# Kernel optimization log

Measured on AMD Instinct MI355X. Metric: run time of the kernel, lower is better.

Reference implementation:

```python
import jax, jax.numpy as jnp
import numpy as np

B, S, D, H = 1, 2048, 2048, 32
HD = D // H
SCALE = float(HD) ** -0.5


def _rope(x, cos, sin):
    # x: (b, s, h, hd); interleaved-pair RoPE as in executorch apply_rotary_emb
    xr, xi = x[..., 0::2], x[..., 1::2]
    c = cos[None, :, None, :]
    s = sin[None, :, None, :]
    out = jnp.stack([xr * c - xi * s, xr * s + xi * c], axis=-1)
    return out.reshape(x.shape)


def setup_inputs() -> dict:
    key = jax.random.key(0)
    ks = jax.random.split(key, 8)
    hidden_states = jax.random.normal(ks[0], (B, S, D), jnp.float32)
    pos = jnp.arange(S, dtype=jnp.float32)
    inv = 1.0 / (10000.0 ** (jnp.arange(0, HD, 2, dtype=jnp.float32) / HD))
    ang = pos[:, None] * inv[None, :]  # (S, HD//2)
    freqs_cos = jnp.cos(ang)
    freqs_sin = jnp.sin(ang)
    causal = jnp.tril(jnp.ones((S, S), dtype=bool))
    attention_mask = jnp.where(causal, 0.0, -1e9).astype(jnp.float32)[None, None]
    k_cache = jax.random.normal(ks[1], (B, S, H, HD), jnp.float32)
    v_cache = jax.random.normal(ks[2], (B, S, H, HD), jnp.float32)
    k_mask = jnp.ones((B, S, 1, 1), jnp.float32)
    v_mask = jnp.ones((B, S, 1, 1), jnp.float32)
    # weights stored as (in, out); math-equivalent to torch Linear(out,in) @ W.T
    wq = jax.random.normal(ks[3], (D, D), jnp.float32) * 0.02
    wk = jax.random.normal(ks[4], (D, D), jnp.float32) * 0.02
    wv = jax.random.normal(ks[5], (D, D), jnp.float32) * 0.02
    wo = jax.random.normal(ks[6], (D, D), jnp.float32) * 0.02
    return {"hidden_states": hidden_states, "freqs_cos": freqs_cos,
            "freqs_sin": freqs_sin, "attention_mask": attention_mask,
            "k_cache": k_cache, "v_cache": v_cache,
            "k_mask": k_mask, "v_mask": v_mask,
            "wq": wq, "wk": wk, "wv": wv, "wo": wo}


def reference(hidden_states, freqs_cos, freqs_sin, attention_mask,
              k_cache, v_cache, k_mask, v_mask, wq, wk, wv, wo):
    b, s, _ = hidden_states.shape
    q = (hidden_states @ wq).reshape(b, s, H, HD)
    k = (hidden_states @ wk).reshape(b, s, H, HD)
    v = (hidden_states @ wv).reshape(b, s, H, HD)
    q = _rope(q, freqs_cos, freqs_sin)
    k = _rope(k, freqs_cos, freqs_sin)
    # mask-blend KV cache update
    k = k_cache * (1.0 - k_mask) + k * k_mask  # (b, S, H, HD)
    v = v_cache * (1.0 - v_mask) + v * v_mask
    qt = q.transpose(0, 2, 1, 3)  # (b, H, s, HD)
    kt = k.transpose(0, 2, 1, 3)
    vt = v.transpose(0, 2, 1, 3)
    attn = jnp.einsum('bhqd,bhkd->bhqk', qt, kt) * SCALE + attention_mask
    attn = jax.nn.softmax(attn, axis=-1)
    y = jnp.einsum('bhqk,bhkd->bhqd', attn, vt)  # (b, H, s, HD)
    # torch: y.transpose(0,1).contiguous().view(b, s, dim); valid since b == 1
    y = jnp.swapaxes(y, 0, 1).reshape(b, s, D)
    y = y @ wo
    return (y, k, v)
```

## Files before the change

kernel.cpp:

```cpp
#include <hip/hip_runtime.h>
#include <hip/hip_bf16.h>
#include <stdint.h>

typedef __bf16 bf16;
typedef __attribute__((ext_vector_type(8))) __bf16 bf16x8;
typedef __attribute__((ext_vector_type(4))) float f32x4;

#define SEQ 2048
#define DIM 2048
#define NHEAD 32
#define HD 64
#define ATT_SCALE 0.125f

__device__ __forceinline__ void gload16(void* lds, const void* g) {
  __builtin_amdgcn_global_load_lds(
      (const __attribute__((address_space(1))) unsigned int*)g,
      (__attribute__((address_space(3))) unsigned int*)lds, 16, 0, 0);
}

__device__ __forceinline__ f32x4 mfma16(bf16x8 a, bf16x8 b, f32x4 c) {
  return __builtin_amdgcn_mfma_f32_16x16x32_bf16(a, b, c, 0, 0, 0);
}

__global__ __launch_bounds__(256) void cvt_hs(const float* __restrict__ in,
                                              bf16* __restrict__ out) {
  size_t i = ((size_t)blockIdx.x * 256 + threadIdx.x) * 8;
  f32x4 a = *(const f32x4*)(in + i);
  f32x4 b = *(const f32x4*)(in + i + 4);
  bf16x8 o;
#pragma unroll
  for (int j = 0; j < 4; ++j) { o[j] = (bf16)a[j]; o[j + 4] = (bf16)b[j]; }
  *(bf16x8*)(out + i) = o;
}

__global__ __launch_bounds__(256) void wtrans(
    const float* __restrict__ w0, const float* __restrict__ w1,
    const float* __restrict__ w2, const float* __restrict__ w3,
    bf16* __restrict__ t0, bf16* __restrict__ t1,
    bf16* __restrict__ t2, bf16* __restrict__ t3) {
  const float* wsrc[4] = {w0, w1, w2, w3};
  bf16* wdst[4] = {t0, t1, t2, t3};
  const float* w = wsrc[blockIdx.z];
  bf16* wT = wdst[blockIdx.z];
  __shared__ alignas(16) bf16 tile[64][72];
  int t = threadIdx.x;
  int n0 = blockIdx.x * 64, k0 = blockIdx.y * 64;
#pragma unroll
  for (int i = 0; i < 4; ++i) {
    int r = (t >> 4) + 16 * i;
    int c = (t & 15) * 4;
    f32x4 v = *(const f32x4*)(w + (size_t)(k0 + r) * DIM + n0 + c);
#pragma unroll
    for (int j = 0; j < 4; ++j) tile[r][c + j] = (bf16)v[j];
  }
  __syncthreads();
#pragma unroll
  for (int i = 0; i < 2; ++i) {
    int n = (t >> 3) + 32 * i;
    int kb = (t & 7) * 8;
    bf16x8 o;
#pragma unroll
    for (int j = 0; j < 8; ++j) o[j] = tile[kb + j][n];
    *(bf16x8*)(wT + (size_t)(n0 + n) * DIM + k0 + kb) = o;
  }
}

template <typename OutT>
__global__ __launch_bounds__(256) void gemm128(
    const bf16* __restrict__ A,
    const bf16* __restrict__ B0, const bf16* __restrict__ B1, const bf16* __restrict__ B2,
    OutT* __restrict__ C0, OutT* __restrict__ C1, OutT* __restrict__ C2,
    int M, int N, int K) {
  const bf16* Bt; OutT* C;
  if (blockIdx.z == 0)      { Bt = B0; C = C0; }
  else if (blockIdx.z == 1) { Bt = B1; C = C1; }
  else                      { Bt = B2; C = C2; }
  __shared__ alignas(16) bf16 As[128][64];
  __shared__ alignas(16) bf16 Bs[128][64];
  int tid = threadIdx.x, lane = tid & 63, w = tid >> 6;
  int wr = w >> 1, wc = w & 1;
  size_t mBase = (size_t)blockIdx.y * 128, nBase = (size_t)blockIdx.x * 128;
  f32x4 acc[4][4] = {};
  int r0 = tid >> 3, sl = tid & 7;
  int lr = lane & 15, hi = lane >> 4, sw = lr & 7;
  for (int kt = 0; kt < K; kt += 64) {
#pragma unroll
    for (int i = 0; i < 4; ++i) {
      int row = r0 + 32 * i;
      int kc = sl ^ (row & 7);
      gload16(&As[row][sl * 8], A + (mBase + row) * K + kt + kc * 8);
      gload16(&Bs[row][sl * 8], Bt + (nBase + row) * K + kt + kc * 8);
    }
    __syncthreads();
#pragma unroll
    for (int kk = 0; kk < 2; ++kk) {
      int cb = kk * 4 + hi;
      bf16x8 a[4], b[4];
#pragma unroll
      for (int m = 0; m < 4; ++m)
        a[m] = *(const bf16x8*)&As[wr * 64 + m * 16 + lr][(cb ^ sw) * 8];
#pragma unroll
      for (int n = 0; n < 4; ++n)
        b[n] = *(const bf16x8*)&Bs[wc * 64 + n * 16 + lr][(cb ^ sw) * 8];
#pragma unroll
      for (int m = 0; m < 4; ++m)
#pragma unroll
        for (int n = 0; n < 4; ++n)
          acc[m][n] = mfma16(a[m], b[n], acc[m][n]);
    }
    __syncthreads();
  }
#pragma unroll
  for (int m = 0; m < 4; ++m)
#pragma unroll
    for (int n = 0; n < 4; ++n)
#pragma unroll
      for (int j = 0; j < 4; ++j) {
        size_t row = mBase + wr * 64 + m * 16 + hi * 4 + j;
        size_t col = nBase + wc * 64 + n * 16 + lr;
        C[row * N + col] = (OutT)acc[m][n][j];
      }
}

__global__ __launch_bounds__(256) void gemm_osk(
    const bf16* __restrict__ A, const bf16* __restrict__ Bt,
    float* __restrict__ P0, float* __restrict__ P1) {
  const int K = DIM, N = DIM;
  float* C = blockIdx.z ? P1 : P0;
  int kbeg = blockIdx.z * (K / 2), kend = kbeg + K / 2;
  __shared__ alignas(16) bf16 As[128][64];
  __shared__ alignas(16) bf16 Bs[128][64];
  int tid = threadIdx.x, lane = tid & 63, w = tid >> 6;
  int wr = w >> 1, wc = w & 1;
  size_t mBase = (size_t)blockIdx.y * 128, nBase = (size_t)blockIdx.x * 128;
  f32x4 acc[4][4] = {};
  int r0 = tid >> 3, sl = tid & 7;
  int lr = lane & 15, hi = lane >> 4, sw = lr & 7;
  for (int kt = kbeg; kt < kend; kt += 64) {
#pragma unroll
    for (int i = 0; i < 4; ++i) {
      int row = r0 + 32 * i;
      int kc = sl ^ (row & 7);
      gload16(&As[row][sl * 8], A + (mBase + row) * K + kt + kc * 8);
      gload16(&Bs[row][sl * 8], Bt + (nBase + row) * K + kt + kc * 8);
    }
    __syncthreads();
#pragma unroll
    for (int kk = 0; kk < 2; ++kk) {
      int cb = kk * 4 + hi;
      bf16x8 a[4], b[4];
#pragma unroll
      for (int m = 0; m < 4; ++m)
        a[m] = *(const bf16x8*)&As[wr * 64 + m * 16 + lr][(cb ^ sw) * 8];
#pragma unroll
      for (int n = 0; n < 4; ++n)
        b[n] = *(const bf16x8*)&Bs[wc * 64 + n * 16 + lr][(cb ^ sw) * 8];
#pragma unroll
      for (int m = 0; m < 4; ++m)
#pragma unroll
        for (int n = 0; n < 4; ++n)
          acc[m][n] = mfma16(a[m], b[n], acc[m][n]);
    }
    __syncthreads();
  }
#pragma unroll
  for (int m = 0; m < 4; ++m)
#pragma unroll
    for (int n = 0; n < 4; ++n)
#pragma unroll
      for (int j = 0; j < 4; ++j) {
        size_t row = mBase + wr * 64 + m * 16 + hi * 4 + j;
        size_t col = nBase + wc * 64 + n * 16 + lr;
        C[row * N + col] = acc[m][n][j];
      }
}

__global__ __launch_bounds__(256) void addp(const float* __restrict__ a,
                                            const float* __restrict__ b,
                                            float* __restrict__ y) {
  size_t i = ((size_t)blockIdx.x * 256 + threadIdx.x) * 4;
  f32x4 va = *(const f32x4*)(a + i);
  f32x4 vb = *(const f32x4*)(b + i);
  *(f32x4*)(y + i) = va + vb;
}

__global__ __launch_bounds__(256) void ropeqk(
    const bf16* __restrict__ qraw, const bf16* __restrict__ kraw,
    const float* __restrict__ fc, const float* __restrict__ fs,
    const float* __restrict__ kcache, const float* __restrict__ kmask,
    float* __restrict__ kout, bf16* __restrict__ qb, bf16* __restrict__ kb) {
  int s = blockIdx.x;
  float km = kmask[s];
  float omk = 1.0f - km;
  for (int p = threadIdx.x; p < DIM / 2; p += 256) {
    int h = p >> 5, i = p & 31;
    float c = fc[s * 32 + i], sn = fs[s * 32 + i];
    size_t src = (size_t)s * DIM + h * 64 + 2 * i;
    float xr = (float)qraw[src], xi = (float)qraw[src + 1];
    float q0v = xr * c - xi * sn, q1v = xr * sn + xi * c;
    size_t dsth = (size_t)h * SEQ * HD + (size_t)s * HD + 2 * i;
    qb[dsth] = (bf16)q0v; qb[dsth + 1] = (bf16)q1v;
    xr = (float)kraw[src]; xi = (float)kraw[src + 1];
    float k0v = xr * c - xi * sn, k1v = xr * sn + xi * c;
    float b0 = kcache[src] * omk + k0v * km;
    float b1 = kcache[src + 1] * omk + k1v * km;
    kout[src] = b0; kout[src + 1] = b1;
    kb[dsth] = (bf16)b0; kb[dsth + 1] = (bf16)b1;
  }
}

__global__ __launch_bounds__(256) void vprep(
    const bf16* __restrict__ vraw, const float* __restrict__ vcache,
    const float* __restrict__ vmask, float* __restrict__ vout,
    bf16* __restrict__ vtb) {
  int h = blockIdx.y;
  int s0 = blockIdx.x * 64;
  __shared__ alignas(16) bf16 tile[64][72];
  int t = threadIdx.x;
#pragma unroll
  for (int i = 0; i < 4; ++i) {
    int r = (t >> 4) + 16 * i;
    int c = (t & 15) * 4;
    int s = s0 + r;
    float vm = vmask[s], om = 1.0f - vm;
    size_t src = (size_t)s * DIM + h * 64 + c;
    f32x4 vc = *(const f32x4*)(vcache + src);
    f32x4 o;
#pragma unroll
    for (int j = 0; j < 4; ++j) {
      float val = vc[j] * om + (float)vraw[src + j] * vm;
      o[j] = val;
      tile[r][c + j] = (bf16)val;
    }
    *(f32x4*)(vout + src) = o;
  }
  __syncthreads();
#pragma unroll
  for (int i = 0; i < 2; ++i) {
    int hd = (t >> 3) + 32 * i;
    int cb = (t & 7) * 8;
    bf16x8 o;
#pragma unroll
    for (int j = 0; j < 8; ++j) o[j] = tile[cb + j][hd];
    *(bf16x8*)(vtb + (size_t)h * HD * SEQ + (size_t)hd * SEQ + s0 + cb) = o;
  }
}

__global__ __launch_bounds__(256) void attn_fwd(
    const bf16* __restrict__ qb, const bf16* __restrict__ kb,
    const bf16* __restrict__ vtb, bf16* __restrict__ ob) {
  int h = blockIdx.y;
  int qt = (h & 1) ? (31 - (int)blockIdx.x) : (int)blockIdx.x;
  int q0 = qt * 64;
  __shared__ alignas(16) bf16 Ks[2][64][64];
  __shared__ alignas(16) bf16 Vs[2][64][64];
  __shared__ alignas(16) bf16 Ps[4][16][64];
  int tid = threadIdx.x, lane = tid & 63, w = tid >> 6;
  const bf16* qh = qb + (size_t)h * SEQ * HD;
  const bf16* kh = kb + (size_t)h * SEQ * HD;
  const bf16* vh = vtb + (size_t)h * HD * SEQ;
  int lr = lane & 15, hi = lane >> 4, sw = lr & 7;
  int qrow = q0 + w * 16 + lr;
  bf16x8 qf[2];
#pragma unroll
  for (int kk = 0; kk < 2; ++kk)
    qf[kk] = *(const bf16x8*)(qh + (size_t)qrow * HD + kk * 32 + hi * 8);
  f32x4 ot[4] = {};
  float mrun = -3e38f, lrun = 0.f;
  int nt = qt + 1;
  int r0 = tid >> 3, sl = tid & 7;
  char* PsW = (char*)&Ps[w][0][0];

  auto STAGE = [&](int t, int b) {
    int kv0 = t * 64;
#pragma unroll
    for (int i = 0; i < 2; ++i) {
      int row = r0 + 32 * i;
      int kc = sl ^ (row & 7);
      gload16(&Ks[b][row][sl * 8], kh + (size_t)(kv0 + row) * HD + kc * 8);
      gload16(&Vs[b][row][sl * 8], vh + (size_t)row * SEQ + kv0 + kc * 8);
    }
  };

  STAGE(0, 0);
  int buf = 0;
  for (int t = 0; t < nt; ++t) {
    __syncthreads();
    if (t + 1 < nt) STAGE(t + 1, buf ^ 1);
    int kv0 = t * 64;
    f32x4 st[4] = {};
    __builtin_amdgcn_s_setprio(1);
#pragma unroll
    for (int kk = 0; kk < 2; ++kk) {
      int cb = kk * 4 + hi;
#pragma unroll
      for (int n = 0; n < 4; ++n) {
        bf16x8 kf = *(const bf16x8*)&Ks[buf][n * 16 + lr][(cb ^ sw) * 8];
        st[n] = mfma16(kf, qf[kk], st[n]);
      }
    }
    __builtin_amdgcn_s_setprio(0);
    float tmax = -3e38f;
    if (t == nt - 1) {
#pragma unroll
      for (int n = 0; n < 4; ++n)
#pragma unroll
        for (int j = 0; j < 4; ++j) {
          int key = kv0 + n * 16 + hi * 4 + j;
          float v = (key <= qrow) ? st[n][j] * ATT_SCALE : -1e30f;
          st[n][j] = v;
          tmax = fmaxf(tmax, v);
        }
    } else {
#pragma unroll
      for (int n = 0; n < 4; ++n)
#pragma unroll
        for (int j = 0; j < 4; ++j) {
          float v = st[n][j] * ATT_SCALE;
          st[n][j] = v;
          tmax = fmaxf(tmax, v);
        }
    }
    tmax = fmaxf(tmax, __shfl_xor(tmax, 16));
    tmax = fmaxf(tmax, __shfl_xor(tmax, 32));
    float mnew = fmaxf(mrun, tmax);
    float psum = 0.f;
    if (__all(tmax <= mrun)) {
#pragma unroll
      for (int n = 0; n < 4; ++n)
#pragma unroll
        for (int j = 0; j < 4; ++j) {
          float p = __expf(st[n][j] - mrun);
          st[n][j] = p;
          psum += p;
        }
      psum += __shfl_xor(psum, 16);
      psum += __shfl_xor(psum, 32);
      lrun += psum;
    } else {
      float alpha = __expf(mrun - mnew);
#pragma unroll
      for (int n = 0; n < 4; ++n)
#pragma unroll
        for (int j = 0; j < 4; ++j) {
          float p = __expf(st[n][j] - mnew);
          st[n][j] = p;
          psum += p;
        }
      psum += __shfl_xor(psum, 16);
      psum += __shfl_xor(psum, 32);
      lrun = lrun * alpha + psum;
      mrun = mnew;
#pragma unroll
      for (int nd = 0; nd < 4; ++nd)
#pragma unroll
        for (int j = 0; j < 4; ++j) ot[nd][j] *= alpha;
    }
#pragma unroll
    for (int n = 0; n < 4; ++n) {
      union { bf16 b[4]; uint2 u; } pk;
#pragma unroll
      for (int j = 0; j < 4; ++j) pk.b[j] = (bf16)st[n][j];
      int keyc = n * 2 + (hi >> 1);
      *(uint2*)(PsW + lr * 128 + ((keyc ^ sw) * 16) + (hi & 1) * 8) = pk.u;
    }
    __builtin_amdgcn_s_setprio(1);
#pragma unroll
    for (int kk = 0; kk < 2; ++kk) {
      int cb = kk * 4 + hi;
      bf16x8 pf = *(const bf16x8*)(PsW + lr * 128 + ((cb ^ sw) * 16));
#pragma unroll
      for (int nd = 0; nd < 4; ++nd) {
        bf16x8 vf = *(const bf16x8*)&Vs[buf][nd * 16 + lr][(cb ^ sw) * 8];
        ot[nd] = mfma16(vf, pf, ot[nd]);
      }
    }
    __builtin_amdgcn_s_setprio(0);
    buf ^= 1;
  }
  float rinv = 1.0f / lrun;
  bf16* orow = ob + ((size_t)h * SEQ + qrow) * HD;
#pragma unroll
  for (int nd = 0; nd < 4; ++nd) {
    union { bf16 b[4]; uint2 u; } o;
#pragma unroll
    for (int j = 0; j < 4; ++j) o.b[j] = (bf16)(ot[nd][j] * rinv);
    *(uint2*)(orow + nd * 16 + hi * 4) = o.u;
  }
}

extern "C" void kernel_launch(void* const* d_in, const int* in_sizes, int n_in,
                              void* d_out, int out_size, void* d_ws, size_t ws_size,
                              hipStream_t stream) {
  const float* hs     = (const float*)d_in[0];
  const float* fc     = (const float*)d_in[1];
  const float* fs     = (const float*)d_in[2];
  const float* kcache = (const float*)d_in[4];
  const float* vcache = (const float*)d_in[5];
  const float* kmask  = (const float*)d_in[6];
  const float* vmask  = (const float*)d_in[7];
  const float* wq     = (const float*)d_in[8];
  const float* wk     = (const float*)d_in[9];
  const float* wv     = (const float*)d_in[10];
  const float* wo     = (const float*)d_in[11];

  float* y    = (float*)d_out;
  float* kout = y + (size_t)SEQ * DIM;
  float* vout = y + 2 * (size_t)SEQ * DIM;

  char* ws = (char*)d_ws;
  const size_t MB8 = (size_t)SEQ * DIM * sizeof(bf16);
  bf16* wqT  = (bf16*)(ws + 0 * MB8);
  bf16* wkT  = (bf16*)(ws + 1 * MB8);
  bf16* wvT  = (bf16*)(ws + 2 * MB8);
  bf16* woT  = (bf16*)(ws + 3 * MB8);
  bf16* hsb  = (bf16*)(ws + 4 * MB8);
  bf16* qraw = (bf16*)(ws + 5 * MB8);
  bf16* kraw = (bf16*)(ws + 6 * MB8);
  bf16* vraw = (bf16*)(ws + 7 * MB8);
  bf16* qb   = (bf16*)(ws + 8 * MB8);
  bf16* kb   = (bf16*)(ws + 9 * MB8);
  bf16* vtb  = (bf16*)(ws + 10 * MB8);
  bf16* ob   = hsb;
  float* p0 = (float*)(ws + 5 * MB8);
  float* p1 = (float*)(ws + 7 * MB8);

  cvt_hs<<<dim3(SEQ * DIM / 2048), dim3(256), 0, stream>>>(hs, hsb);
  wtrans<<<dim3(32, 32, 4), dim3(256), 0, stream>>>(wq, wk, wv, wo, wqT, wkT, wvT, woT);
  gemm128<bf16><<<dim3(16, 16, 3), dim3(256), 0, stream>>>(
      hsb, wqT, wkT, wvT, qraw, kraw, vraw, SEQ, DIM, DIM);
  ropeqk<<<dim3(SEQ), dim3(256), 0, stream>>>(qraw, kraw, fc, fs, kcache, kmask, kout, qb, kb);
  vprep<<<dim3(32, 32), dim3(256), 0, stream>>>(vraw, vcache, vmask, vout, vtb);
  attn_fwd<<<dim3(32, NHEAD), dim3(256), 0, stream>>>(qb, kb, vtb, ob);
  gemm_osk<<<dim3(16, 16, 2), dim3(256), 0, stream>>>(ob, woT, p0, p1);
  addp<<<dim3(SEQ * DIM / 1024), dim3(256), 0, stream>>>(p0, p1, y);
}
```

Measured before the change: 221.6 us.

## Pair complementary causal query tiles per attention block to share K/V loads

Each attention block now handles two query tiles, qp and 31-qp, of the same head. The K/V tiles loaded into LDS feed both tiles' QK and PV MFMAs. Every block therefore gets the same amount of causal work, global and LDS traffic for K/V is shared, and the grid halves to 512 blocks. The cost is roughly double the accumulator and Q registers, more LDS for a second P buffer, and branches on doA inside the loop, which could lower occupancy.

```diff
diff --git a/kernel.cpp b/kernel.cpp
--- a/kernel.cpp
+++ b/kernel.cpp
@@ -249,27 +249,33 @@
 __global__ __launch_bounds__(256) void attn_fwd(
     const bf16* __restrict__ qb, const bf16* __restrict__ kb,
     const bf16* __restrict__ vtb, bf16* __restrict__ ob) {
-  int h = blockIdx.y;
-  int qt = (h & 1) ? (31 - (int)blockIdx.x) : (int)blockIdx.x;
-  int q0 = qt * 64;
+  int p = blockIdx.x;
+  int h = p & 31;
+  int qp = p >> 5;
+  int qtA = qp, qtB = 31 - qp;
   __shared__ alignas(16) bf16 Ks[2][64][64];
   __shared__ alignas(16) bf16 Vs[2][64][64];
-  __shared__ alignas(16) bf16 Ps[4][16][64];
+  __shared__ alignas(16) bf16 PsA[4][16][64];
+  __shared__ alignas(16) bf16 PsB[4][16][64];
   int tid = threadIdx.x, lane = tid & 63, w = tid >> 6;
   const bf16* qh = qb + (size_t)h * SEQ * HD;
   const bf16* kh = kb + (size_t)h * SEQ * HD;
   const bf16* vh = vtb + (size_t)h * HD * SEQ;
   int lr = lane & 15, hi = lane >> 4, sw = lr & 7;
-  int qrow = q0 + w * 16 + lr;
-  bf16x8 qf[2];
-#pragma unroll
-  for (int kk = 0; kk < 2; ++kk)
-    qf[kk] = *(const bf16x8*)(qh + (size_t)qrow * HD + kk * 32 + hi * 8);
-  f32x4 ot[4] = {};
-  float mrun = -3e38f, lrun = 0.f;
-  int nt = qt + 1;
+  int qrowA = qtA * 64 + w * 16 + lr;
+  int qrowB = qtB * 64 + w * 16 + lr;
+  bf16x8 qfA[2], qfB[2];
+#pragma unroll
+  for (int kk = 0; kk < 2; ++kk) {
+    qfA[kk] = *(const bf16x8*)(qh + (size_t)qrowA * HD + kk * 32 + hi * 8);
+    qfB[kk] = *(const bf16x8*)(qh + (size_t)qrowB * HD + kk * 32 + hi * 8);
+  }
+  f32x4 otA[4] = {}, otB[4] = {};
+  float mA = -3e38f, lA = 0.f, mB = -3e38f, lB = 0.f;
+  int ntA = qtA + 1, ntB = qtB + 1;
   int r0 = tid >> 3, sl = tid & 7;
-  char* PsW = (char*)&Ps[w][0][0];
+  char* PsWA = (char*)&PsA[w][0][0];
+  char* PsWB = (char*)&PsB[w][0][0];
 
   auto STAGE = [&](int t, int b) {
     int kv0 = t * 64;
@@ -282,26 +288,10 @@
     }
   };
 
-  STAGE(0, 0);
-  int buf = 0;
-  for (int t = 0; t < nt; ++t) {
-    __syncthreads();
-    if (t + 1 < nt) STAGE(t + 1, buf ^ 1);
-    int kv0 = t * 64;
-    f32x4 st[4] = {};
-    __builtin_amdgcn_s_setprio(1);
-#pragma unroll
-    for (int kk = 0; kk < 2; ++kk) {
-      int cb = kk * 4 + hi;
-#pragma unroll
-      for (int n = 0; n < 4; ++n) {
-        bf16x8 kf = *(const bf16x8*)&Ks[buf][n * 16 + lr][(cb ^ sw) * 8];
-        st[n] = mfma16(kf, qf[kk], st[n]);
-      }
-    }
-    __builtin_amdgcn_s_setprio(0);
+  auto SOFTMAX = [&](f32x4* st, float& mrun, float& lrun, f32x4* ot,
+                     bool last, int kv0, int qrow, char* PsW) {
     float tmax = -3e38f;
-    if (t == nt - 1) {
+    if (last) {
 #pragma unroll
       for (int n = 0; n < 4; ++n)
 #pragma unroll
@@ -330,9 +320,9 @@
       for (int n = 0; n < 4; ++n)
 #pragma unroll
         for (int j = 0; j < 4; ++j) {
-          float p = __expf(st[n][j] - mrun);
-          st[n][j] = p;
-          psum += p;
+          float pv = __expf(st[n][j] - mrun);
+          st[n][j] = pv;
+          psum += pv;
         }
       psum += __shfl_xor(psum, 16);
       psum += __shfl_xor(psum, 32);
@@ -343,9 +333,9 @@
       for (int n = 0; n < 4; ++n)
 #pragma unroll
         for (int j = 0; j < 4; ++j) {
-          float p = __expf(st[n][j] - mnew);
-          st[n][j] = p;
-          psum += p;
+          float pv = __expf(st[n][j] - mnew);
+          st[n][j] = pv;
+          psum += pv;
         }
       psum += __shfl_xor(psum, 16);
       psum += __shfl_xor(psum, 32);
@@ -364,28 +354,59 @@
       int keyc = n * 2 + (hi >> 1);
       *(uint2*)(PsW + lr * 128 + ((keyc ^ sw) * 16) + (hi & 1) * 8) = pk.u;
     }
+  };
+
+  STAGE(0, 0);
+  int buf = 0;
+  for (int t = 0; t < ntB; ++t) {
+    __syncthreads();
+    if (t + 1 < ntB) STAGE(t + 1, buf ^ 1);
+    int kv0 = t * 64;
+    bool doA = (t < ntA);
+    f32x4 stA[4] = {}, stB[4] = {};
     __builtin_amdgcn_s_setprio(1);
 #pragma unroll
     for (int kk = 0; kk < 2; ++kk) {
       int cb = kk * 4 + hi;
-      bf16x8 pf = *(const bf16x8*)(PsW + lr * 128 + ((cb ^ sw) * 16));
+#pragma unroll
+      for (int n = 0; n < 4; ++n) {
+        bf16x8 kf = *(const bf16x8*)&Ks[buf][n * 16 + lr][(cb ^ sw) * 8];
+        if (doA) stA[n] = mfma16(kf, qfA[kk], stA[n]);
+        stB[n] = mfma16(kf, qfB[kk], stB[n]);
+      }
+    }
+    __builtin_amdgcn_s_setprio(0);
+    if (doA) SOFTMAX(stA, mA, lA, otA, t == ntA - 1, kv0, qrowA, PsWA);
+    SOFTMAX(stB, mB, lB, otB, t == ntB - 1, kv0, qrowB, PsWB);
+    __builtin_amdgcn_s_setprio(1);
+#pragma unroll
+    for (int kk = 0; kk < 2; ++kk) {
+      int cb = kk * 4 + hi;
+      bf16x8 pfA = *(const bf16x8*)(PsWA + lr * 128 + ((cb ^ sw) * 16));
+      bf16x8 pfB = *(const bf16x8*)(PsWB + lr * 128 + ((cb ^ sw) * 16));
 #pragma unroll
       for (int nd = 0; nd < 4; ++nd) {
         bf16x8 vf = *(const bf16x8*)&Vs[buf][nd * 16 + lr][(cb ^ sw) * 8];
-        ot[nd] = mfma16(vf, pf, ot[nd]);
+        if (doA) otA[nd] = mfma16(vf, pfA, otA[nd]);
+        otB[nd] = mfma16(vf, pfB, otB[nd]);
       }
     }
     __builtin_amdgcn_s_setprio(0);
     buf ^= 1;
   }
-  float rinv = 1.0f / lrun;
-  bf16* orow = ob + ((size_t)h * SEQ + qrow) * HD;
+  float rA = 1.0f / lA, rB = 1.0f / lB;
+  bf16* orowA = ob + ((size_t)h * SEQ + qrowA) * HD;
+  bf16* orowB = ob + ((size_t)h * SEQ + qrowB) * HD;
 #pragma unroll
   for (int nd = 0; nd < 4; ++nd) {
-    union { bf16 b[4]; uint2 u; } o;
-#pragma unroll
-    for (int j = 0; j < 4; ++j) o.b[j] = (bf16)(ot[nd][j] * rinv);
-    *(uint2*)(orow + nd * 16 + hi * 4) = o.u;
+    union { bf16 b[4]; uint2 u; } oa, obk;
+#pragma unroll
+    for (int j = 0; j < 4; ++j) {
+      oa.b[j] = (bf16)(otA[nd][j] * rA);
+      obk.b[j] = (bf16)(otB[nd][j] * rB);
+    }
+    *(uint2*)(orowA + nd * 16 + hi * 4) = oa.u;
+    *(uint2*)(orowB + nd * 16 + hi * 4) = obk.u;
   }
 }
 
@@ -431,7 +452,7 @@
       hsb, wqT, wkT, wvT, qraw, kraw, vraw, SEQ, DIM, DIM);
   ropeqk<<<dim3(SEQ), dim3(256), 0, stream>>>(qraw, kraw, fc, fs, kcache, kmask, kout, qb, kb);
   vprep<<<dim3(32, 32), dim3(256), 0, stream>>>(vraw, vcache, vmask, vout, vtb);
-  attn_fwd<<<dim3(32, NHEAD), dim3(256), 0, stream>>>(qb, kb, vtb, ob);
+  attn_fwd<<<dim3(512), dim3(256), 0, stream>>>(qb, kb, vtb, ob);
   gemm_osk<<<dim3(16, 16, 2), dim3(256), 0, stream>>>(ob, woT, p0, p1);
   addp<<<dim3(SEQ * DIM / 1024), dim3(256), 0, stream>>>(p0, p1, y);
 }
```

Result: slower. 247.3 us (+11.6%).

## Pair causal query tiles per workgroup for balanced attention work

Applied to the files above, without the earlier changes.

The attention kernel now gives each workgroup two query tiles (qp and 31-qp) of the same head, so every workgroup processes exactly 33 KV tiles instead of 1 to 32. The grid shrinks from 1024 to 512 workgroups, and the block index is remapped so that consecutive workgroups spread across XCDs. This removes the causal load imbalance and tail effect, at the cost of fewer workgroups (less occupancy slack) and more registers for the two sets of accumulators.

```diff
diff --git a/kernel.cpp b/kernel.cpp
--- a/kernel.cpp
+++ b/kernel.cpp
@@ -249,9 +249,13 @@
 __global__ __launch_bounds__(256) void attn_fwd(
     const bf16* __restrict__ qb, const bf16* __restrict__ kb,
     const bf16* __restrict__ vtb, bf16* __restrict__ ob) {
-  int h = blockIdx.y;
-  int qt = (h & 1) ? (31 - (int)blockIdx.x) : (int)blockIdx.x;
-  int q0 = qt * 64;
+  int orig = blockIdx.x;
+  int wg = (orig & 7) * 64 + (orig >> 3);
+  int h = wg >> 4;
+  int qp = wg & 15;
+  int qtA = qp, qtB = 31 - qp;
+  int ntA = qtA + 1;
+  const int NT = 33;
   __shared__ alignas(16) bf16 Ks[2][64][64];
   __shared__ alignas(16) bf16 Vs[2][64][64];
   __shared__ alignas(16) bf16 Ps[4][16][64];
@@ -260,19 +264,20 @@
   const bf16* kh = kb + (size_t)h * SEQ * HD;
   const bf16* vh = vtb + (size_t)h * HD * SEQ;
   int lr = lane & 15, hi = lane >> 4, sw = lr & 7;
-  int qrow = q0 + w * 16 + lr;
-  bf16x8 qf[2];
-#pragma unroll
-  for (int kk = 0; kk < 2; ++kk)
-    qf[kk] = *(const bf16x8*)(qh + (size_t)qrow * HD + kk * 32 + hi * 8);
-  f32x4 ot[4] = {};
-  float mrun = -3e38f, lrun = 0.f;
-  int nt = qt + 1;
+  int qrowA = qtA * 64 + w * 16 + lr;
+  int qrowB = qtB * 64 + w * 16 + lr;
+  bf16x8 qfA[2], qfB[2];
+#pragma unroll
+  for (int kk = 0; kk < 2; ++kk) {
+    qfA[kk] = *(const bf16x8*)(qh + (size_t)qrowA * HD + kk * 32 + hi * 8);
+    qfB[kk] = *(const bf16x8*)(qh + (size_t)qrowB * HD + kk * 32 + hi * 8);
+  }
+  f32x4 otA[4] = {}, otB[4] = {};
+  float mA = -3e38f, lA = 0.f, mB = -3e38f, lB = 0.f;
   int r0 = tid >> 3, sl = tid & 7;
   char* PsW = (char*)&Ps[w][0][0];
 
-  auto STAGE = [&](int t, int b) {
-    int kv0 = t * 64;
+  auto STAGE = [&](int kv0, int b) {
 #pragma unroll
     for (int i = 0; i < 2; ++i) {
       int row = r0 + 32 * i;
@@ -282,12 +287,8 @@
     }
   };
 
-  STAGE(0, 0);
-  int buf = 0;
-  for (int t = 0; t < nt; ++t) {
-    __syncthreads();
-    if (t + 1 < nt) STAGE(t + 1, buf ^ 1);
-    int kv0 = t * 64;
+  auto BODY = [&](int buf, int kv0, bf16x8 (&qf)[2], f32x4 (&ot)[4],
+                  float& mrun, float& lrun, int qrow, bool last) {
     f32x4 st[4] = {};
     __builtin_amdgcn_s_setprio(1);
 #pragma unroll
@@ -301,7 +302,7 @@
     }
     __builtin_amdgcn_s_setprio(0);
     float tmax = -3e38f;
-    if (t == nt - 1) {
+    if (last) {
 #pragma unroll
       for (int n = 0; n < 4; ++n)
 #pragma unroll
@@ -330,9 +331,9 @@
       for (int n = 0; n < 4; ++n)
 #pragma unroll
         for (int j = 0; j < 4; ++j) {
-          float p = __expf(st[n][j] - mrun);
-          st[n][j] = p;
-          psum += p;
+          float pv = __expf(st[n][j] - mrun);
+          st[n][j] = pv;
+          psum += pv;
         }
       psum += __shfl_xor(psum, 16);
       psum += __shfl_xor(psum, 32);
@@ -343,9 +344,9 @@
       for (int n = 0; n < 4; ++n)
 #pragma unroll
         for (int j = 0; j < 4; ++j) {
-          float p = __expf(st[n][j] - mnew);
-          st[n][j] = p;
-          psum += p;
+          float pv = __expf(st[n][j] - mnew);
+          st[n][j] = pv;
+          psum += pv;
         }
       psum += __shfl_xor(psum, 16);
       psum += __shfl_xor(psum, 32);
@@ -376,17 +377,40 @@
       }
     }
     __builtin_amdgcn_s_setprio(0);
+  };
+
+  auto STORE = [&](f32x4 (&ot)[4], float lrun, int qrow) {
+    float rinv = 1.0f / lrun;
+    bf16* orow = ob + ((size_t)h * SEQ + qrow) * HD;
+#pragma unroll
+    for (int nd = 0; nd < 4; ++nd) {
+      union { bf16 b[4]; uint2 u; } o;
+#pragma unroll
+      for (int j = 0; j < 4; ++j) o.b[j] = (bf16)(ot[nd][j] * rinv);
+      *(uint2*)(orow + nd * 16 + hi * 4) = o.u;
+    }
+  };
+
+  STAGE(0, 0);
+  int buf = 0;
+  for (int t = 0; t < NT; ++t) {
+    __syncthreads();
+    if (t + 1 < NT) {
+      int tn = t + 1;
+      int kvn = (tn < ntA ? tn : tn - ntA) * 64;
+      STAGE(kvn, buf ^ 1);
+    }
+    if (t < ntA) {
+      int kv0 = t * 64;
+      BODY(buf, kv0, qfA, otA, mA, lA, qrowA, t == ntA - 1);
+      if (t == ntA - 1) STORE(otA, lA, qrowA);
+    } else {
+      int kv0 = (t - ntA) * 64;
+      BODY(buf, kv0, qfB, otB, mB, lB, qrowB, t == NT - 1);
+    }
     buf ^= 1;
   }
-  float rinv = 1.0f / lrun;
-  bf16* orow = ob + ((size_t)h * SEQ + qrow) * HD;
-#pragma unroll
-  for (int nd = 0; nd < 4; ++nd) {
-    union { bf16 b[4]; uint2 u; } o;
-#pragma unroll
-    for (int j = 0; j < 4; ++j) o.b[j] = (bf16)(ot[nd][j] * rinv);
-    *(uint2*)(orow + nd * 16 + hi * 4) = o.u;
-  }
+  STORE(otB, lB, qrowB);
 }
 
 extern "C" void kernel_launch(void* const* d_in, const int* in_sizes, int n_in,
@@ -431,7 +455,7 @@
       hsb, wqT, wkT, wvT, qraw, kraw, vraw, SEQ, DIM, DIM);
   ropeqk<<<dim3(SEQ), dim3(256), 0, stream>>>(qraw, kraw, fc, fs, kcache, kmask, kout, qb, kb);
   vprep<<<dim3(32, 32), dim3(256), 0, stream>>>(vraw, vcache, vmask, vout, vtb);
-  attn_fwd<<<dim3(32, NHEAD), dim3(256), 0, stream>>>(qb, kb, vtb, ob);
+  attn_fwd<<<dim3(512), dim3(256), 0, stream>>>(qb, kb, vtb, ob);
   gemm_osk<<<dim3(16, 16, 2), dim3(256), 0, stream>>>(ob, woT, p0, p1);
   addp<<<dim3(SEQ * DIM / 1024), dim3(256), 0, stream>>>(p0, p1, y);
 }
```

Result: faster. 200.0 us (-9.7%).
